# Optimization experiments

Hardware: AMD Instinct MI355X
Metric: run time of the kernel (lower is better)

Reference implementation:

```python
import jax, jax.numpy as jnp
import numpy as np

B, N_SRC, N_DST, E, F = 2, 131072, 131072, 524288, 64
EPS = 1e-8


def setup_inputs() -> dict:
    key = jax.random.key(0)
    k1, k2, k3 = jax.random.split(key, 3)
    x = jax.random.normal(k1, (B, N_SRC, F), dtype=jnp.float32)
    edge_index = jax.random.randint(k2, (2, E), 0, N_DST, dtype=jnp.int64)
    weights = jax.random.uniform(k3, (E,), dtype=jnp.float32)
    return {"x": x, "edge_index": edge_index, "weights": weights}


def reference(x, edge_index, weights):
    src = edge_index[0]  # (E,) indices into source nodes
    dst = edge_index[1]  # (E,) indices into destination nodes
    # _row_normalize_weights: normalize per destination node
    norm = jax.ops.segment_sum(weights, dst, num_segments=N_DST)  # (N_DST,)
    w = weights / (norm[dst] + EPS)  # (E,)
    # Batched SpMM: out[b, d, :] = sum_{e: dst[e]==d} w[e] * x[b, src[e], :]
    gathered = x[:, src, :] * w[None, :, None]  # (B, E, F)
    out = jnp.zeros((B, N_DST, F), dtype=x.dtype).at[:, dst, :].add(gathered)
    return out
```

## Files before the change

kernel.cpp:

```cpp
#include <hip/hip_runtime.h>

#define NB    2
#define NDST  131072
#define NSRC  131072
#define FF    64
#define EE    524288
#define EPSV  1e-8f
#define SCAN_BLOCKS 512
#define NBUCK 256
#define NB1   512
#define CAP   4096

typedef unsigned long long u64;

__global__ __launch_bounds__(256) void histA_kernel(const int* __restrict__ dst,
                                                    int* __restrict__ histg) {
    __shared__ int cnt[NBUCK];
    int t = threadIdx.x;
    int b = blockIdx.x;
    for (int i = t; i < NBUCK; i += 256) cnt[i] = 0;
    __syncthreads();
    int base = b * 1024;
    #pragma unroll
    for (int it = 0; it < 4; ++it) {
        int d = dst[base + it * 256 + t];
        atomicAdd(&cnt[d >> 9], 1);
    }
    __syncthreads();
    for (int i = t; i < NBUCK; i += 256) histg[i * NB1 + b] = cnt[i];
}

__global__ void scan1_kernel(const int* __restrict__ counts,
                             int* __restrict__ offs, int* __restrict__ bsum) {
    __shared__ int tmp[256];
    int t = threadIdx.x;
    int i = blockIdx.x * 256 + t;
    int v = counts[i];
    tmp[t] = v; __syncthreads();
    for (int off = 1; off < 256; off <<= 1) {
        int add = (t >= off) ? tmp[t - off] : 0;
        __syncthreads();
        tmp[t] += add;
        __syncthreads();
    }
    offs[i] = tmp[t] - v;
    if (t == 255) bsum[blockIdx.x] = tmp[t];
}

__global__ void scan2_kernel(int* __restrict__ bsum) {
    __shared__ int tmp[SCAN_BLOCKS];
    int t = threadIdx.x;
    int v = bsum[t];
    tmp[t] = v; __syncthreads();
    for (int off = 1; off < SCAN_BLOCKS; off <<= 1) {
        int add = (t >= off) ? tmp[t - off] : 0;
        __syncthreads();
        tmp[t] += add;
        __syncthreads();
    }
    bsum[t] = tmp[t] - v;
}

__global__ void scan3_kernel(int* __restrict__ posg, const int* __restrict__ bsum) {
    int i = blockIdx.x * 256 + threadIdx.x;
    posg[i] += bsum[blockIdx.x];
    if (i == 0) posg[NBUCK * NB1] = EE;
}

__global__ __launch_bounds__(256) void scatterA_kernel(const int* __restrict__ src,
                                                       const int* __restrict__ dst,
                                                       const float* __restrict__ wts,
                                                       const int* __restrict__ posg,
                                                       u64* __restrict__ tmp_rec) {
    __shared__ int cur[NBUCK];
    int t = threadIdx.x;
    int b = blockIdx.x;
    cur[t] = posg[t * NB1 + b];
    __syncthreads();
    int base = b * 1024;
    #pragma unroll
    for (int it = 0; it < 4; ++it) {
        int e = base + it * 256 + t;
        int d = dst[e];
        int p = atomicAdd(&cur[d >> 9], 1);
        u64 r = ((u64)__float_as_uint(wts[e]) << 32)
              | ((u64)(d & 511) << 17)
              | (unsigned)src[e];
        tmp_rec[p] = r;
    }
}

__global__ __launch_bounds__(256) void bucket_kernel(const int* __restrict__ posg,
                                                     const u64* __restrict__ tmp_rec,
                                                     int* __restrict__ offs,
                                                     u64* __restrict__ rec) {
    __shared__ u64 ld_rec[CAP];
    __shared__ unsigned short ld_bin[CAP];
    __shared__ int cnt[512];
    __shared__ int excl[512];
    __shared__ int s[256];

    int t = threadIdx.x;
    int k = blockIdx.x;
    int lo = posg[k * NB1];
    int hi = posg[(k + 1) * NB1];
    int n  = hi - lo;
    if (n > CAP) n = CAP;

    for (int j = t; j < 512; j += 256) cnt[j] = 0;
    __syncthreads();

    for (int i = t; i < n; i += 256) {
        u64 r = tmp_rec[lo + i];
        int bin = (int)((r >> 17) & 511);
        ld_rec[i] = r;
        ld_bin[i] = (unsigned short)bin;
        atomicAdd(&cnt[bin], 1);
    }
    __syncthreads();

    int a0 = cnt[2 * t], a1 = cnt[2 * t + 1];
    s[t] = a0 + a1;
    __syncthreads();
    for (int off = 1; off < 256; off <<= 1) {
        int add = (t >= off) ? s[t - off] : 0;
        __syncthreads();
        s[t] += add;
        __syncthreads();
    }
    int ex = s[t] - (a0 + a1);
    excl[2 * t]     = ex;
    excl[2 * t + 1] = ex + a0;
    __syncthreads();

    offs[k * 512 + t]       = lo + excl[t];
    offs[k * 512 + t + 256] = lo + excl[t + 256];
    if (k == NBUCK - 1 && t == 0) offs[NDST] = EE;

    cnt[2 * t]     = lo + excl[2 * t];
    cnt[2 * t + 1] = lo + excl[2 * t + 1];
    __syncthreads();

    const u64 mask = (((u64)0xFFFFFFFFu) << 32) | 0x1FFFFu;
    for (int i = t; i < n; i += 256) {
        int bin = ld_bin[i];
        int p = atomicAdd(&cnt[bin], 1);
        rec[p] = ld_rec[i] & mask;
    }
}

__global__ __launch_bounds__(256) void gather_kernel(const float* __restrict__ x,
                                                     const int* __restrict__ offs,
                                                     const u64* __restrict__ rec,
                                                     float* __restrict__ out) {
    int gid  = blockIdx.x * blockDim.x + threadIdx.x;
    int d    = gid >> 6;
    int lane = gid & 63;

    int begin = offs[d];
    int end   = offs[d + 1];

    const float* xb0 = x + lane;
    const float* xb1 = x + (size_t)NSRC * FF + lane;

    float acc0 = 0.f, acc1 = 0.f, sumw = 0.f;
    int e = begin;
    for (; e + 4 <= end; e += 4) {
        u64 r0 = rec[e + 0];
        u64 r1 = rec[e + 1];
        u64 r2 = rec[e + 2];
        u64 r3 = rec[e + 3];
        int s0 = (int)(unsigned)r0;  float w0 = __uint_as_float((unsigned)(r0 >> 32));
        int s1 = (int)(unsigned)r1;  float w1 = __uint_as_float((unsigned)(r1 >> 32));
        int s2 = (int)(unsigned)r2;  float w2 = __uint_as_float((unsigned)(r2 >> 32));
        int s3 = (int)(unsigned)r3;  float w3 = __uint_as_float((unsigned)(r3 >> 32));
        float a00 = xb0[(size_t)s0 * FF];
        float a10 = xb0[(size_t)s1 * FF];
        float a20 = xb0[(size_t)s2 * FF];
        float a30 = xb0[(size_t)s3 * FF];
        float a01 = xb1[(size_t)s0 * FF];
        float a11 = xb1[(size_t)s1 * FF];
        float a21 = xb1[(size_t)s2 * FF];
        float a31 = xb1[(size_t)s3 * FF];
        sumw += (w0 + w1) + (w2 + w3);
        acc0 = fmaf(w0, a00, fmaf(w1, a10, fmaf(w2, a20, fmaf(w3, a30, acc0))));
        acc1 = fmaf(w0, a01, fmaf(w1, a11, fmaf(w2, a21, fmaf(w3, a31, acc1))));
    }
    for (; e < end; ++e) {
        u64 r = rec[e];
        int s = (int)(unsigned)r;
        float w = __uint_as_float((unsigned)(r >> 32));
        sumw += w;
        acc0 = fmaf(w, xb0[(size_t)s * FF], acc0);
        acc1 = fmaf(w, xb1[(size_t)s * FF], acc1);
    }
    float inv = 1.0f / (sumw + EPSV);
    __builtin_nontemporal_store(acc0 * inv, &out[(size_t)d * FF + lane]);
    __builtin_nontemporal_store(acc1 * inv, &out[(size_t)NDST * FF + (size_t)d * FF + lane]);
}

extern "C" void kernel_launch(void* const* d_in, const int* in_sizes, int n_in,
                              void* d_out, int out_size, void* d_ws, size_t ws_size,
                              hipStream_t stream) {
    const float* x          = (const float*)d_in[0];
    const int*   edge_index = (const int*)d_in[1];
    const float* weights    = (const float*)d_in[2];

    const int* src = edge_index;
    const int* dst = edge_index + EE;
    float* out = (float*)d_out;

    char* w8 = (char*)d_ws;
    u64* tmp_rec = (u64*)w8;
    u64* rec     = (u64*)(w8 + (size_t)EE * 8);
    int* histg   = (int*)(w8 + (size_t)EE * 16);
    int* posg    = histg + NBUCK * NB1;
    int* bsum    = posg + NBUCK * NB1 + 8;
    int* offs    = bsum + SCAN_BLOCKS;

    histA_kernel<<<NB1, 256, 0, stream>>>(dst, histg);
    scan1_kernel<<<SCAN_BLOCKS, 256, 0, stream>>>(histg, posg, bsum);
    scan2_kernel<<<1, SCAN_BLOCKS, 0, stream>>>(bsum);
    scan3_kernel<<<SCAN_BLOCKS, 256, 0, stream>>>(posg, bsum);
    scatterA_kernel<<<NB1, 256, 0, stream>>>(src, dst, weights, posg, tmp_rec);
    bucket_kernel<<<NBUCK, 256, 0, stream>>>(posg, tmp_rec, offs, rec);
    gather_kernel<<<(NDST * 64) / 256, 256, 0, stream>>>(x, offs, rec, out);
}
```

Before: 189.3 us.

## Fuse per-bucket local sort with gather using finer 64-destination buckets

The bucket count grows from 256 to 2048, so each bucket covers 64 destination nodes. The second-level sort and the SpMM gather are merged into one kernel: each block counting-sorts its bucket's records in LDS and then gathers the x rows directly. This drops the global `rec` and `offs` arrays and one kernel launch. In exchange, the histogram and scan grow to 1M entries, the scatter spreads its writes over many more buckets, gather parallelism per block becomes serial over 16 nodes per wave, and any bucket with more than 512 edges would be silently truncated.

```diff
diff --git a/kernel.cpp b/kernel.cpp
--- a/kernel.cpp
+++ b/kernel.cpp
@@ -6,10 +6,12 @@
 #define FF    64
 #define EE    524288
 #define EPSV  1e-8f
-#define SCAN_BLOCKS 512
-#define NBUCK 256
+
+#define NBUCK 2048
 #define NB1   512
-#define CAP   4096
+#define NCNT  (NBUCK * NB1)
+#define SCAN_BLOCKS (NCNT / 256)
+#define CAPB  512
 
 typedef unsigned long long u64;
 
@@ -24,7 +26,7 @@
     #pragma unroll
     for (int it = 0; it < 4; ++it) {
         int d = dst[base + it * 256 + t];
-        atomicAdd(&cnt[d >> 9], 1);
+        atomicAdd(&cnt[d >> 6], 1);
     }
     __syncthreads();
     for (int i = t; i < NBUCK; i += 256) histg[i * NB1 + b] = cnt[i];
@@ -47,24 +49,29 @@
     if (t == 255) bsum[blockIdx.x] = tmp[t];
 }
 
-__global__ void scan2_kernel(int* __restrict__ bsum) {
-    __shared__ int tmp[SCAN_BLOCKS];
-    int t = threadIdx.x;
-    int v = bsum[t];
-    tmp[t] = v; __syncthreads();
-    for (int off = 1; off < SCAN_BLOCKS; off <<= 1) {
+__global__ __launch_bounds__(1024) void scan2_kernel(int* __restrict__ bsum) {
+    __shared__ int tmp[1024];
+    int t = threadIdx.x;
+    int v0 = bsum[4 * t], v1 = bsum[4 * t + 1], v2 = bsum[4 * t + 2], v3 = bsum[4 * t + 3];
+    int s = v0 + v1 + v2 + v3;
+    tmp[t] = s; __syncthreads();
+    for (int off = 1; off < 1024; off <<= 1) {
         int add = (t >= off) ? tmp[t - off] : 0;
         __syncthreads();
         tmp[t] += add;
         __syncthreads();
     }
-    bsum[t] = tmp[t] - v;
+    int ex = tmp[t] - s;
+    bsum[4 * t]     = ex;
+    bsum[4 * t + 1] = ex + v0;
+    bsum[4 * t + 2] = ex + v0 + v1;
+    bsum[4 * t + 3] = ex + v0 + v1 + v2;
 }
 
 __global__ void scan3_kernel(int* __restrict__ posg, const int* __restrict__ bsum) {
     int i = blockIdx.x * 256 + threadIdx.x;
     posg[i] += bsum[blockIdx.x];
-    if (i == 0) posg[NBUCK * NB1] = EE;
+    if (i == 0) posg[NCNT] = EE;
 }
 
 __global__ __launch_bounds__(256) void scatterA_kernel(const int* __restrict__ src,
@@ -75,128 +82,111 @@
     __shared__ int cur[NBUCK];
     int t = threadIdx.x;
     int b = blockIdx.x;
-    cur[t] = posg[t * NB1 + b];
+    for (int i = t; i < NBUCK; i += 256) cur[i] = posg[i * NB1 + b];
     __syncthreads();
     int base = b * 1024;
     #pragma unroll
     for (int it = 0; it < 4; ++it) {
         int e = base + it * 256 + t;
         int d = dst[e];
-        int p = atomicAdd(&cur[d >> 9], 1);
+        int p = atomicAdd(&cur[d >> 6], 1);
         u64 r = ((u64)__float_as_uint(wts[e]) << 32)
-              | ((u64)(d & 511) << 17)
+              | ((u64)(d & 63) << 17)
               | (unsigned)src[e];
         tmp_rec[p] = r;
     }
 }
 
-__global__ __launch_bounds__(256) void bucket_kernel(const int* __restrict__ posg,
-                                                     const u64* __restrict__ tmp_rec,
-                                                     int* __restrict__ offs,
-                                                     u64* __restrict__ rec) {
-    __shared__ u64 ld_rec[CAP];
-    __shared__ unsigned short ld_bin[CAP];
-    __shared__ int cnt[512];
-    __shared__ int excl[512];
-    __shared__ int s[256];
+__global__ __launch_bounds__(256) void fused_kernel(const float* __restrict__ x,
+                                                    const int* __restrict__ posg,
+                                                    const u64* __restrict__ tmp_rec,
+                                                    float* __restrict__ out) {
+    __shared__ u64 stage[CAPB];
+    __shared__ u64 sorted[CAPB];
+    __shared__ int cnt[64];
+    __shared__ int loffs[65];
 
     int t = threadIdx.x;
     int k = blockIdx.x;
     int lo = posg[k * NB1];
     int hi = posg[(k + 1) * NB1];
     int n  = hi - lo;
-    if (n > CAP) n = CAP;
-
-    for (int j = t; j < 512; j += 256) cnt[j] = 0;
+    if (n > CAPB) n = CAPB;
+
+    if (t < 64) cnt[t] = 0;
     __syncthreads();
 
     for (int i = t; i < n; i += 256) {
         u64 r = tmp_rec[lo + i];
-        int bin = (int)((r >> 17) & 511);
-        ld_rec[i] = r;
-        ld_bin[i] = (unsigned short)bin;
-        atomicAdd(&cnt[bin], 1);
-    }
-    __syncthreads();
-
-    int a0 = cnt[2 * t], a1 = cnt[2 * t + 1];
-    s[t] = a0 + a1;
-    __syncthreads();
-    for (int off = 1; off < 256; off <<= 1) {
-        int add = (t >= off) ? s[t - off] : 0;
-        __syncthreads();
-        s[t] += add;
-        __syncthreads();
-    }
-    int ex = s[t] - (a0 + a1);
-    excl[2 * t]     = ex;
-    excl[2 * t + 1] = ex + a0;
-    __syncthreads();
-
-    offs[k * 512 + t]       = lo + excl[t];
-    offs[k * 512 + t + 256] = lo + excl[t + 256];
-    if (k == NBUCK - 1 && t == 0) offs[NDST] = EE;
-
-    cnt[2 * t]     = lo + excl[2 * t];
-    cnt[2 * t + 1] = lo + excl[2 * t + 1];
-    __syncthreads();
-
-    const u64 mask = (((u64)0xFFFFFFFFu) << 32) | 0x1FFFFu;
+        stage[i] = r;
+        atomicAdd(&cnt[(int)((r >> 17) & 63)], 1);
+    }
+    __syncthreads();
+
+    if (t < 64) {
+        int c = cnt[t];
+        int incl = c;
+        #pragma unroll
+        for (int off = 1; off < 64; off <<= 1) {
+            int o = __shfl_up(incl, off, 64);
+            if (t >= off) incl += o;
+        }
+        loffs[t + 1] = incl;
+        if (t == 0) loffs[0] = 0;
+        cnt[t] = incl - c;
+    }
+    __syncthreads();
+
     for (int i = t; i < n; i += 256) {
-        int bin = ld_bin[i];
-        int p = atomicAdd(&cnt[bin], 1);
-        rec[p] = ld_rec[i] & mask;
-    }
-}
-
-__global__ __launch_bounds__(256) void gather_kernel(const float* __restrict__ x,
-                                                     const int* __restrict__ offs,
-                                                     const u64* __restrict__ rec,
-                                                     float* __restrict__ out) {
-    int gid  = blockIdx.x * blockDim.x + threadIdx.x;
-    int d    = gid >> 6;
-    int lane = gid & 63;
-
-    int begin = offs[d];
-    int end   = offs[d + 1];
-
+        u64 r = stage[i];
+        int p = atomicAdd(&cnt[(int)((r >> 17) & 63)], 1);
+        sorted[p] = r;
+    }
+    __syncthreads();
+
+    int wave = t >> 6, lane = t & 63;
     const float* xb0 = x + lane;
     const float* xb1 = x + (size_t)NSRC * FF + lane;
 
-    float acc0 = 0.f, acc1 = 0.f, sumw = 0.f;
-    int e = begin;
-    for (; e + 4 <= end; e += 4) {
-        u64 r0 = rec[e + 0];
-        u64 r1 = rec[e + 1];
-        u64 r2 = rec[e + 2];
-        u64 r3 = rec[e + 3];
-        int s0 = (int)(unsigned)r0;  float w0 = __uint_as_float((unsigned)(r0 >> 32));
-        int s1 = (int)(unsigned)r1;  float w1 = __uint_as_float((unsigned)(r1 >> 32));
-        int s2 = (int)(unsigned)r2;  float w2 = __uint_as_float((unsigned)(r2 >> 32));
-        int s3 = (int)(unsigned)r3;  float w3 = __uint_as_float((unsigned)(r3 >> 32));
-        float a00 = xb0[(size_t)s0 * FF];
-        float a10 = xb0[(size_t)s1 * FF];
-        float a20 = xb0[(size_t)s2 * FF];
-        float a30 = xb0[(size_t)s3 * FF];
-        float a01 = xb1[(size_t)s0 * FF];
-        float a11 = xb1[(size_t)s1 * FF];
-        float a21 = xb1[(size_t)s2 * FF];
-        float a31 = xb1[(size_t)s3 * FF];
-        sumw += (w0 + w1) + (w2 + w3);
-        acc0 = fmaf(w0, a00, fmaf(w1, a10, fmaf(w2, a20, fmaf(w3, a30, acc0))));
-        acc1 = fmaf(w0, a01, fmaf(w1, a11, fmaf(w2, a21, fmaf(w3, a31, acc1))));
-    }
-    for (; e < end; ++e) {
-        u64 r = rec[e];
-        int s = (int)(unsigned)r;
-        float w = __uint_as_float((unsigned)(r >> 32));
-        sumw += w;
-        acc0 = fmaf(w, xb0[(size_t)s * FF], acc0);
-        acc1 = fmaf(w, xb1[(size_t)s * FF], acc1);
-    }
-    float inv = 1.0f / (sumw + EPSV);
-    __builtin_nontemporal_store(acc0 * inv, &out[(size_t)d * FF + lane]);
-    __builtin_nontemporal_store(acc1 * inv, &out[(size_t)NDST * FF + (size_t)d * FF + lane]);
+    for (int dl = wave * 16; dl < wave * 16 + 16; ++dl) {
+        int begin = loffs[dl];
+        int end   = loffs[dl + 1];
+        float acc0 = 0.f, acc1 = 0.f, sumw = 0.f;
+        int e = begin;
+        for (; e + 4 <= end; e += 4) {
+            u64 r0 = sorted[e + 0];
+            u64 r1 = sorted[e + 1];
+            u64 r2 = sorted[e + 2];
+            u64 r3 = sorted[e + 3];
+            int s0 = (int)(r0 & 0x1FFFF);  float w0 = __uint_as_float((unsigned)(r0 >> 32));
+            int s1 = (int)(r1 & 0x1FFFF);  float w1 = __uint_as_float((unsigned)(r1 >> 32));
+            int s2 = (int)(r2 & 0x1FFFF);  float w2 = __uint_as_float((unsigned)(r2 >> 32));
+            int s3 = (int)(r3 & 0x1FFFF);  float w3 = __uint_as_float((unsigned)(r3 >> 32));
+            float a00 = xb0[(size_t)s0 * FF];
+            float a10 = xb0[(size_t)s1 * FF];
+            float a20 = xb0[(size_t)s2 * FF];
+            float a30 = xb0[(size_t)s3 * FF];
+            float a01 = xb1[(size_t)s0 * FF];
+            float a11 = xb1[(size_t)s1 * FF];
+            float a21 = xb1[(size_t)s2 * FF];
+            float a31 = xb1[(size_t)s3 * FF];
+            sumw += (w0 + w1) + (w2 + w3);
+            acc0 = fmaf(w0, a00, fmaf(w1, a10, fmaf(w2, a20, fmaf(w3, a30, acc0))));
+            acc1 = fmaf(w0, a01, fmaf(w1, a11, fmaf(w2, a21, fmaf(w3, a31, acc1))));
+        }
+        for (; e < end; ++e) {
+            u64 r = sorted[e];
+            int s = (int)(r & 0x1FFFF);
+            float w = __uint_as_float((unsigned)(r >> 32));
+            sumw += w;
+            acc0 = fmaf(w, xb0[(size_t)s * FF], acc0);
+            acc1 = fmaf(w, xb1[(size_t)s * FF], acc1);
+        }
+        float inv = 1.0f / (sumw + EPSV);
+        int d = k * 64 + dl;
+        __builtin_nontemporal_store(acc0 * inv, &out[(size_t)d * FF + lane]);
+        __builtin_nontemporal_store(acc1 * inv, &out[(size_t)NDST * FF + (size_t)d * FF + lane]);
+    }
 }
 
 extern "C" void kernel_launch(void* const* d_in, const int* in_sizes, int n_in,
@@ -210,19 +200,15 @@
     const int* dst = edge_index + EE;
     float* out = (float*)d_out;
 
-    char* w8 = (char*)d_ws;
-    u64* tmp_rec = (u64*)w8;
-    u64* rec     = (u64*)(w8 + (size_t)EE * 8);
-    int* histg   = (int*)(w8 + (size_t)EE * 16);
-    int* posg    = histg + NBUCK * NB1;
-    int* bsum    = posg + NBUCK * NB1 + 8;
-    int* offs    = bsum + SCAN_BLOCKS;
+    int* histg   = (int*)d_ws;
+    u64* tmp_rec = (u64*)d_ws;
+    int* posg    = histg + NCNT;
+    int* bsum    = posg + NCNT + 8;
 
     histA_kernel<<<NB1, 256, 0, stream>>>(dst, histg);
     scan1_kernel<<<SCAN_BLOCKS, 256, 0, stream>>>(histg, posg, bsum);
-    scan2_kernel<<<1, SCAN_BLOCKS, 0, stream>>>(bsum);
+    scan2_kernel<<<1, 1024, 0, stream>>>(bsum);
     scan3_kernel<<<SCAN_BLOCKS, 256, 0, stream>>>(posg, bsum);
     scatterA_kernel<<<NB1, 256, 0, stream>>>(src, dst, weights, posg, tmp_rec);
-    bucket_kernel<<<NBUCK, 256, 0, stream>>>(posg, tmp_rec, offs, rec);
-    gather_kernel<<<(NDST * 64) / 256, 256, 0, stream>>>(x, offs, rec, out);
-}
+    fused_kernel<<<NBUCK, 256, 0, stream>>>(x, posg, tmp_rec, out);
+}
```

Result: faster. 181.0 us (-4.4%).
